# Kernel optimization log

Measured on AMD Instinct MI355X. Metric: run time of the kernel, lower is better.

Reference implementation:

```python
import jax, jax.numpy as jnp
import numpy as np

EMBED_CHOICES = (512, 768, 1024)
RATIO_CHOICES = (2, 3, 4)
D_MAX = 1024           # max embed_dim
H_MAX = 4096           # max expansion dim = 1024 * 4


def setup_inputs() -> dict:
    key = jax.random.key(0)
    ks = jax.random.split(key, 7)
    return {
        "x": jax.random.normal(ks[0], (8, 512, D_MAX), dtype=jnp.float32),
        "w0": jax.random.normal(ks[1], (H_MAX, D_MAX), dtype=jnp.float32) * 0.02,
        "b0": jax.random.normal(ks[2], (H_MAX,), dtype=jnp.float32) * 0.02,
        "w1": jax.random.normal(ks[3], (D_MAX, H_MAX), dtype=jnp.float32) * 0.02,
        "b1": jax.random.normal(ks[4], (D_MAX,), dtype=jnp.float32) * 0.02,
        "arch_embed": jax.random.normal(ks[5], (3,), dtype=jnp.float32),
        "arch_mlp": jax.random.normal(ks[6], (3,), dtype=jnp.float32),
    }


def _effective_masks(a, b):
    """Weighted-sum-of-sliced-linears == single linear with masked effective weights.

    Candidate (e, r): uses W0[:e*r, :e] on x[..., :e], zero-padded to H_MAX,
    and W1[:e, :e*r] on h[..., :e*r], zero-padded to D_MAX.
    """
    col = jnp.arange(D_MAX)
    row = jnp.arange(H_MAX)
    m0 = jnp.zeros((H_MAX, D_MAX), dtype=jnp.float32)
    bm0 = jnp.zeros((H_MAX,), dtype=jnp.float32)
    m1 = jnp.zeros((D_MAX, H_MAX), dtype=jnp.float32)
    bm1 = jnp.zeros((D_MAX,), dtype=jnp.float32)
    for ie, e in enumerate(EMBED_CHOICES):
        cm = (col < e).astype(jnp.float32)          # [D_MAX]
        for ir, r in enumerate(RATIO_CHOICES):
            w = a[ie] * b[ir]
            rm = (row < e * r).astype(jnp.float32)  # [H_MAX]
            m0 = m0 + w * rm[:, None] * cm[None, :]
            bm0 = bm0 + w * rm
            m1 = m1 + w * cm[:, None] * rm[None, :]
            bm1 = bm1 + w * cm
    return m0, bm0, m1, bm1


def reference(x, w0, b0, w1, b1, arch_embed, arch_mlp):
    a = jax.nn.softmax(arch_embed)  # DARTS-style arch weights over embed_dim
    b = jax.nn.softmax(arch_mlp)    # over mlp_ratio
    m0, bm0, m1, bm1 = _effective_masks(a, b)
    # layer 0 mix: [B,S,D] @ [D,H] -> [B,S,H]
    h = jnp.einsum("bsd,hd->bsh", x, m0 * w0) + bm0 * b0
    h = jax.nn.relu(h)
    # layer 1 mix: [B,S,H] @ [H,D] -> [B,S,D]
    out = jnp.einsum("bsh,dh->bsd", h, m1 * w1) + bm1 * b1
    # dropout p=0.0 (eval): identity
    return out
```

## Files before the change

### kernel.cpp

```cpp
#include <hip/hip_runtime.h>


typedef __attribute__((ext_vector_type(8))) short bf16x8;
typedef __attribute__((ext_vector_type(4))) float f32x4;
typedef __attribute__((ext_vector_type(8))) unsigned short u16x8;

#define AS1 __attribute__((address_space(1)))
#define AS3 __attribute__((address_space(3)))

__device__ __forceinline__ unsigned short f2bf(float f) {
  unsigned int x = __float_as_uint(f);
  x += 0x7fffu + ((x >> 16) & 1u);
  return (unsigned short)(x >> 16);
}

__device__ __forceinline__ void softmax3(const float* __restrict__ p, float* o) {
  float m = fmaxf(p[0], fmaxf(p[1], p[2]));
  float e0 = expf(p[0] - m), e1 = expf(p[1] - m), e2 = expf(p[2] - m);
  float inv = 1.0f / (e0 + e1 + e2);
  o[0] = e0 * inv; o[1] = e1 * inv; o[2] = e2 * inv;
}

__device__ __forceinline__ float sval(int h, int d, const float a[3], const float b[3]) {
  constexpr int E[3] = {512, 768, 1024};
  constexpr int R[3] = {2, 3, 4};
  float s = 0.f;
#pragma unroll
  for (int ie = 0; ie < 3; ++ie) {
    if (d < E[ie]) {
      float t = 0.f;
#pragma unroll
      for (int ir = 0; ir < 3; ++ir)
        if (h < E[ie] * R[ir]) t += b[ir];
      s += a[ie] * t;
    }
  }
  return s;
}


__device__ __forceinline__ void cvt8(const float* __restrict__ src,
                                     unsigned short* __restrict__ dst,
                                     size_t base, float s) {
  const f32x4* p = (const f32x4*)(src + base);
  f32x4 v0 = p[0], v1 = p[1];
  u16x8 r;
#pragma unroll
  for (int j = 0; j < 4; ++j) { r[j] = f2bf(v0[j] * s); r[4 + j] = f2bf(v1[j] * s); }
  *(u16x8*)(dst + base) = r;
}

__global__ __launch_bounds__(256) void conv_all(const float* __restrict__ x,
                                                const float* __restrict__ w0,
                                                const float* __restrict__ b0,
                                                const float* __restrict__ w1,
                                                const float* __restrict__ b1,
                                                const float* __restrict__ ae,
                                                const float* __restrict__ am,
                                                unsigned short* __restrict__ xb,
                                                unsigned short* __restrict__ w0e,
                                                unsigned short* __restrict__ w1e,
                                                float* __restrict__ bb0,
                                                float* __restrict__ bb1) {
  int t = blockIdx.x * 256 + threadIdx.x;
  float a[3], b[3];
  softmax3(ae, a); softmax3(am, b);
  if (t < 524288) {
    cvt8(x, xb, (size_t)t * 8, 1.0f);
  } else if (t < 1048576) {
    int base = (t - 524288) * 8;
    cvt8(w0, w0e, base, sval(base >> 10, base & 1023, a, b));
  } else if (t < 1572864) {
    int base = (t - 1048576) * 8;
    cvt8(w1, w1e, base, sval(base & 4095, base >> 12, a, b));
  } else if (t < 1573504) {
    int base = (t - 1572864) * 8;
#pragma unroll
    for (int j = 0; j < 8; ++j) {
      int i = base + j;
      if (i < 4096) bb0[i] = sval(i, 0, a, b) * b0[i];
      else          bb1[i - 4096] = sval(0, i - 4096, a, b) * b1[i - 4096];
    }
  }
}


template <int MODE>
__global__ __launch_bounds__(512, 2) void gemm256(const unsigned short* __restrict__ A,
                                                  const unsigned short* __restrict__ B,
                                                  const float* __restrict__ bias,
                                                  void* __restrict__ Cout,
                                                  int M, int N, int K, int Ksub) {
  extern __shared__ unsigned short lds[];

  const int tid  = threadIdx.x;
  const int lane = tid & 63;
  const int wid  = tid >> 6;
  const int m0   = blockIdx.x * 256;
  const int n0   = blockIdx.y * 256;
  const int wm   = (wid >> 2) * 128;
  const int wn   = (wid & 3) * 64;
  const int kbeg = (MODE == 2) ? blockIdx.z * Ksub : 0;
  const int nt   = Ksub >> 6;

  f32x4 acc[8][4] = {};

  const int srow   = tid >> 2;
  const int schunk = (tid & 3) ^ ((tid >> 3) & 3);
  const unsigned short* Ag = A + (size_t)(m0 + srow) * K + schunk * 8;
  const unsigned short* Bg = B + (size_t)(n0 + srow) * K + schunk * 8;
  const size_t rstep = (size_t)128 * K;

  auto stage2 = [&](int ldsbase, const unsigned short* g, int k) {
    unsigned short* d = lds + ldsbase + tid * 8;
    __builtin_amdgcn_global_load_lds((const AS1 void*)(g + k),
                                     (AS3 void*)d, 16, 0, 0);
    __builtin_amdgcn_global_load_lds((const AS1 void*)(g + rstep + k),
                                     (AS3 void*)(d + 4096), 16, 0, 0);
  };

  const int rc = ((lane >> 4) * 8) ^ (((lane >> 1) & 3) << 3);
  const int ra = (lane & 15) * 32 + rc;

  stage2(0, Ag, kbeg);
  stage2(32768, Bg, kbeg);
  stage2(8192, Ag, kbeg + 32);
  stage2(32768 + 8192, Bg, kbeg + 32);

  int buf = 0;
  for (int T = 0; T < nt; ++T) {
    const int kn = kbeg + T * 64 + 64;
    const bool pf = (T + 1 < nt);
    bf16x8 af[4], bfr[4];
    const int ab  = buf * 2 * 8192;
    const int bbq = 32768 + buf * 2 * 8192;
    const int nb  = (buf ^ 1) * 2 * 8192;

    asm volatile("s_waitcnt vmcnt(4)" ::: "memory");
    __builtin_amdgcn_s_barrier();
    asm volatile("" ::: "memory");
#pragma unroll
    for (int n = 0; n < 4; ++n) bfr[n] = *(const bf16x8*)&lds[bbq + (wn + n * 16) * 32 + ra];
#pragma unroll
    for (int m = 0; m < 4; ++m) af[m] = *(const bf16x8*)&lds[ab + (wm + m * 16) * 32 + ra];
    if (pf) stage2(nb, Ag, kn);
    __builtin_amdgcn_s_barrier();
    asm volatile("" ::: "memory");
    __builtin_amdgcn_s_setprio(1);
#pragma unroll
    for (int m = 0; m < 4; ++m)
#pragma unroll
      for (int n = 0; n < 4; ++n)
        acc[m][n] = __builtin_amdgcn_mfma_f32_16x16x32_bf16(af[m], bfr[n], acc[m][n], 0, 0, 0);
    __builtin_amdgcn_s_setprio(0);

    __builtin_amdgcn_s_barrier();
    asm volatile("" ::: "memory");
#pragma unroll
    for (int m = 0; m < 4; ++m) af[m] = *(const bf16x8*)&lds[ab + (wm + 64 + m * 16) * 32 + ra];
    if (pf) stage2(32768 + nb, Bg, kn);
    __builtin_amdgcn_s_barrier();
    asm volatile("" ::: "memory");
    __builtin_amdgcn_s_setprio(1);
#pragma unroll
    for (int m = 0; m < 4; ++m)
#pragma unroll
      for (int n = 0; n < 4; ++n)
        acc[4 + m][n] = __builtin_amdgcn_mfma_f32_16x16x32_bf16(af[m], bfr[n], acc[4 + m][n], 0, 0, 0);
    __builtin_amdgcn_s_setprio(0);

    if (pf) { asm volatile("s_waitcnt vmcnt(4)" ::: "memory"); }
    else    { asm volatile("s_waitcnt vmcnt(0)" ::: "memory"); }
    __builtin_amdgcn_s_barrier();
    asm volatile("" ::: "memory");
#pragma unroll
    for (int n = 0; n < 4; ++n) bfr[n] = *(const bf16x8*)&lds[bbq + 8192 + (wn + n * 16) * 32 + ra];
#pragma unroll
    for (int m = 0; m < 4; ++m) af[m] = *(const bf16x8*)&lds[ab + 8192 + (wm + m * 16) * 32 + ra];
    if (pf) stage2(nb + 8192, Ag, kn + 32);
    __builtin_amdgcn_s_barrier();
    asm volatile("" ::: "memory");
    __builtin_amdgcn_s_setprio(1);
#pragma unroll
    for (int m = 0; m < 4; ++m)
#pragma unroll
      for (int n = 0; n < 4; ++n)
        acc[m][n] = __builtin_amdgcn_mfma_f32_16x16x32_bf16(af[m], bfr[n], acc[m][n], 0, 0, 0);
    __builtin_amdgcn_s_setprio(0);

    __builtin_amdgcn_s_barrier();
    asm volatile("" ::: "memory");
#pragma unroll
    for (int m = 0; m < 4; ++m) af[m] = *(const bf16x8*)&lds[ab + 8192 + (wm + 64 + m * 16) * 32 + ra];
    if (pf) stage2(32768 + nb + 8192, Bg, kn + 32);
    __builtin_amdgcn_s_barrier();
    asm volatile("" ::: "memory");
    __builtin_amdgcn_s_setprio(1);
#pragma unroll
    for (int m = 0; m < 4; ++m)
#pragma unroll
      for (int n = 0; n < 4; ++n)
        acc[4 + m][n] = __builtin_amdgcn_mfma_f32_16x16x32_bf16(af[m], bfr[n], acc[4 + m][n], 0, 0, 0);
    __builtin_amdgcn_s_setprio(0);

    buf ^= 1;
  }

  const int crow = (lane >> 4) * 4;
  const int ccol = lane & 15;
#pragma unroll
  for (int mi = 0; mi < 8; ++mi) {
#pragma unroll
    for (int n = 0; n < 4; ++n) {
      const int gr = m0 + wm + mi * 16 + crow;
      const int gc = n0 + wn + n * 16 + ccol;
      if (MODE == 0) {
        const float bv = bias[gc];
        unsigned short* H = (unsigned short*)Cout;
#pragma unroll
        for (int r = 0; r < 4; ++r) {
          float v = fmaxf(acc[mi][n][r] + bv, 0.f);
          H[(size_t)(gr + r) * N + gc] = f2bf(v);
        }
      } else if (MODE == 1) {
        const float bv = bias[gc];
        float* C = (float*)Cout;
#pragma unroll
        for (int r = 0; r < 4; ++r)
          C[(size_t)(gr + r) * N + gc] = acc[mi][n][r] + bv;
      } else {
        float* P = (float*)Cout + (size_t)blockIdx.z * M * N;
#pragma unroll
        for (int r = 0; r < 4; ++r)
          P[(size_t)(gr + r) * N + gc] = acc[mi][n][r];
      }
    }
  }
}

__global__ __launch_bounds__(256) void reduce_k(const float* __restrict__ P,
                                                const float* __restrict__ bb1,
                                                float* __restrict__ out,
                                                int n4) {
  const f32x4* p = (const f32x4*)P;
  const f32x4* bv = (const f32x4*)bb1;
  f32x4* o = (f32x4*)out;
  for (int i = blockIdx.x * 256 + threadIdx.x; i < n4; i += gridDim.x * 256) {
    f32x4 v = p[i];
    v += p[i + n4];
    v += p[i + 2 * n4];
    v += p[i + 3 * n4];
    v += bv[i & 255];
    o[i] = v;
  }
}


extern "C" void kernel_launch(void* const* d_in, const int* in_sizes, int n_in,
                              void* d_out, int out_size, void* d_ws, size_t ws_size,
                              hipStream_t stream) {
  const float* x  = (const float*)d_in[0];
  const float* w0 = (const float*)d_in[1];
  const float* b0 = (const float*)d_in[2];
  const float* w1 = (const float*)d_in[3];
  const float* b1 = (const float*)d_in[4];
  const float* ae = (const float*)d_in[5];
  const float* am = (const float*)d_in[6];

  char* ws = (char*)d_ws;
  unsigned short* xb   = (unsigned short*)(ws);
  unsigned short* w0e  = (unsigned short*)(ws + (8u  << 20));
  unsigned short* w1e  = (unsigned short*)(ws + (16u << 20));
  unsigned short* Hbuf = (unsigned short*)(ws + (24u << 20));
  float* bb0 = (float*)(ws + (56u << 20));
  float* bb1 = (float*)(ws + (56u << 20) + 16384);
  float* part = (float*)(ws + (57u << 20));
  const size_t WS_NEEDED = (57u << 20) + (64u << 20);

  conv_all<<<6147, 256, 0, stream>>>(x, w0, b0, w1, b1, ae, am,
                                     xb, w0e, w1e, bb0, bb1);

  dim3 g1(16, 16);
  gemm256<0><<<g1, 512, 131072, stream>>>(xb, w0e, bb0, Hbuf, 4096, 4096, 1024, 1024);

  if (ws_size >= WS_NEEDED) {
    dim3 g2(16, 4, 4);
    gemm256<2><<<g2, 512, 131072, stream>>>(Hbuf, w1e, nullptr, part, 4096, 1024, 4096, 1024);
    reduce_k<<<2048, 256, 0, stream>>>(part, bb1, (float*)d_out, 1024 * 1024);
  } else {
    dim3 g2(16, 4);
    gemm256<1><<<g2, 512, 131072, stream>>>(Hbuf, w1e, bb1, d_out, 4096, 1024, 4096, 4096);
  }
}
```

Baseline: 189.4 us.

## Use 128x128 split-K=2 GEMM for second layer and XCD-aware tile remap

Replaces the second-layer 256x256 split-K=4 GEMM with a new 128x128-tile kernel using split-K=2, giving 512 blocks instead of 256 and halving the partial-sum traffic reduced afterwards. Both GEMMs remap block indices so that tiles dispatched to the same XCD share A/B rows, improving L2 locality. The reduce kernel now sums two partials, and the workspace requirement shrinks. Smaller tiles lower arithmetic intensity per block and add LDS reloads.

```diff
diff --git a/kernel.cpp b/kernel.cpp
--- a/kernel.cpp
+++ b/kernel.cpp
@@ -96,8 +96,14 @@
   const int tid  = threadIdx.x;
   const int lane = tid & 63;
   const int wid  = tid >> 6;
-  const int m0   = blockIdx.x * 256;
-  const int n0   = blockIdx.y * 256;
+  int bx = blockIdx.x, by = blockIdx.y;
+  if (MODE == 0) {
+    int lb = by * 16 + bx, xcd = lb & 7, p = lb >> 3;
+    bx = (xcd & 1) * 8 + (p & 7);
+    by = (xcd >> 1) * 4 + (p >> 3);
+  }
+  const int m0   = bx * 256;
+  const int n0   = by * 256;
   const int wm   = (wid >> 2) * 128;
   const int wn   = (wid & 3) * 64;
   const int kbeg = (MODE == 2) ? blockIdx.z * Ksub : 0;
@@ -236,6 +242,114 @@
       }
     }
   }
+}
+
+
+__global__ __launch_bounds__(256, 2) void gemm128p(const unsigned short* __restrict__ A,
+                                                   const unsigned short* __restrict__ B,
+                                                   float* __restrict__ P,
+                                                   int M, int N, int K, int Ksub) {
+  __shared__ unsigned short lds[32768];
+
+  const int tid  = threadIdx.x;
+  const int lane = tid & 63;
+  const int wid  = tid >> 6;
+  int lb = blockIdx.y * 32 + blockIdx.x, xcd = lb & 7, p = lb >> 3;
+  const int bx = (xcd & 3) * 8 + (p & 7);
+  const int by = (xcd >> 2) * 4 + (p >> 3);
+  const int m0   = bx * 128;
+  const int n0   = by * 128;
+  const int wm   = (wid >> 1) * 64;
+  const int wn   = (wid & 1) * 64;
+  const int kbeg = blockIdx.z * Ksub;
+  const int nt   = Ksub >> 6;
+
+  f32x4 acc[4][4] = {};
+
+  const int srow   = tid >> 2;
+  const int schunk = (tid & 3) ^ ((tid >> 3) & 3);
+  const unsigned short* Ag = A + (size_t)(m0 + srow) * K + schunk * 8;
+  const unsigned short* Bg = B + (size_t)(n0 + srow) * K + schunk * 8;
+  const size_t rstep = (size_t)64 * K;
+
+  auto stage2 = [&](int ldsbase, const unsigned short* g, int k) {
+    unsigned short* d = lds + ldsbase + tid * 8;
+    __builtin_amdgcn_global_load_lds((const AS1 void*)(g + k),
+                                     (AS3 void*)d, 16, 0, 0);
+    __builtin_amdgcn_global_load_lds((const AS1 void*)(g + rstep + k),
+                                     (AS3 void*)(d + 2048), 16, 0, 0);
+  };
+
+  const int rc = ((lane >> 4) * 8) ^ (((lane >> 1) & 3) << 3);
+  const int ra = (lane & 15) * 32 + rc;
+
+  stage2(0, Ag, kbeg);
+  stage2(16384, Bg, kbeg);
+  stage2(4096, Ag, kbeg + 32);
+  stage2(16384 + 4096, Bg, kbeg + 32);
+
+  int buf = 0;
+  for (int T = 0; T < nt; ++T) {
+    const int kn = kbeg + T * 64 + 64;
+    const bool pf = (T + 1 < nt);
+    bf16x8 af[4], bfr[4];
+    const int ab  = buf * 2 * 4096;
+    const int bbq = 16384 + buf * 2 * 4096;
+    const int nb  = (buf ^ 1) * 2 * 4096;
+
+    asm volatile("s_waitcnt vmcnt(4)" ::: "memory");
+    __builtin_amdgcn_s_barrier();
+    asm volatile("" ::: "memory");
+#pragma unroll
+    for (int n = 0; n < 4; ++n) bfr[n] = *(const bf16x8*)&lds[bbq + (wn + n * 16) * 32 + ra];
+#pragma unroll
+    for (int m = 0; m < 4; ++m) af[m] = *(const bf16x8*)&lds[ab + (wm + m * 16) * 32 + ra];
+    if (pf) { stage2(nb, Ag, kn); stage2(16384 + nb, Bg, kn); }
+    __builtin_amdgcn_s_barrier();
+    asm volatile("" ::: "memory");
+    __builtin_amdgcn_s_setprio(1);
+#pragma unroll
+    for (int m = 0; m < 4; ++m)
+#pragma unroll
+      for (int n = 0; n < 4; ++n)
+        acc[m][n] = __builtin_amdgcn_mfma_f32_16x16x32_bf16(af[m], bfr[n], acc[m][n], 0, 0, 0);
+    __builtin_amdgcn_s_setprio(0);
+
+    if (pf) { asm volatile("s_waitcnt vmcnt(4)" ::: "memory"); }
+    else    { asm volatile("s_waitcnt vmcnt(0)" ::: "memory"); }
+    __builtin_amdgcn_s_barrier();
+    asm volatile("" ::: "memory");
+#pragma unroll
+    for (int n = 0; n < 4; ++n) bfr[n] = *(const bf16x8*)&lds[bbq + 4096 + (wn + n * 16) * 32 + ra];
+#pragma unroll
+    for (int m = 0; m < 4; ++m) af[m] = *(const bf16x8*)&lds[ab + 4096 + (wm + m * 16) * 32 + ra];
+    if (pf) { stage2(nb + 4096, Ag, kn + 32); stage2(16384 + nb + 4096, Bg, kn + 32); }
+    __builtin_amdgcn_s_barrier();
+    asm volatile("" ::: "memory");
+    __builtin_amdgcn_s_setprio(1);
+#pragma unroll
+    for (int m = 0; m < 4; ++m)
+#pragma unroll
+      for (int n = 0; n < 4; ++n)
+        acc[m][n] = __builtin_amdgcn_mfma_f32_16x16x32_bf16(af[m], bfr[n], acc[m][n], 0, 0, 0);
+    __builtin_amdgcn_s_setprio(0);
+
+    buf ^= 1;
+  }
+
+  const int crow = (lane >> 4) * 4;
+  const int ccol = lane & 15;
+  float* Pz = P + (size_t)blockIdx.z * M * N;
+#pragma unroll
+  for (int m = 0; m < 4; ++m)
+#pragma unroll
+    for (int n = 0; n < 4; ++n) {
+      const int gr = m0 + wm + m * 16 + crow;
+      const int gc = n0 + wn + n * 16 + ccol;
+#pragma unroll
+      for (int r = 0; r < 4; ++r)
+        Pz[(size_t)(gr + r) * N + gc] = acc[m][n][r];
+    }
 }
 
 __global__ __launch_bounds__(256) void reduce_k(const float* __restrict__ P,
@@ -248,8 +362,6 @@
   for (int i = blockIdx.x * 256 + threadIdx.x; i < n4; i += gridDim.x * 256) {
     f32x4 v = p[i];
     v += p[i + n4];
-    v += p[i + 2 * n4];
-    v += p[i + 3 * n4];
     v += bv[i & 255];
     o[i] = v;
   }
@@ -275,7 +387,7 @@
   float* bb0 = (float*)(ws + (56u << 20));
   float* bb1 = (float*)(ws + (56u << 20) + 16384);
   float* part = (float*)(ws + (57u << 20));
-  const size_t WS_NEEDED = (57u << 20) + (64u << 20);
+  const size_t WS_NEEDED = (57u << 20) + (32u << 20);
 
   conv_all<<<6147, 256, 0, stream>>>(x, w0, b0, w1, b1, ae, am,
                                      xb, w0e, w1e, bb0, bb1);
@@ -284,9 +396,9 @@
   gemm256<0><<<g1, 512, 131072, stream>>>(xb, w0e, bb0, Hbuf, 4096, 4096, 1024, 1024);
 
   if (ws_size >= WS_NEEDED) {
-    dim3 g2(16, 4, 4);
-    gemm256<2><<<g2, 512, 131072, stream>>>(Hbuf, w1e, nullptr, part, 4096, 1024, 4096, 1024);
-    reduce_k<<<2048, 256, 0, stream>>>(part, bb1, (float*)d_out, 1024 * 1024);
+    dim3 g2(32, 8, 2);
+    gemm128p<<<g2, 256, 0, stream>>>(Hbuf, w1e, part, 4096, 1024, 4096, 2048);
+    reduce_k<<<2048, 256, 0, stream>>>(part, bb1, (float*)d_out, 1048576);
   } else {
     dim3 g2(16, 4);
     gemm256<1><<<g2, 512, 131072, stream>>>(Hbuf, w1e, bb1, d_out, 4096, 1024, 4096, 4096);
```

New measurement: 188.6 us. About the same (-0.4%).
